# Kernel tuning notes

Measured on AMD Instinct MI355X. Metric: run time of the kernel, lower is better.

Reference implementation:

```python
import jax, jax.numpy as jnp
import numpy as np

B, S, DIM = 2, 2048, 2048
H = 16
KV_RANK = 512          # rank_lora_kv
NOPE, ROPE, VDIM = 128, 64, 128
QK = NOPE + ROPE       # 192
SCALE = QK ** -0.5     # seq <= original_seq_len so YaRN mscale = 1
THETA = 10000.0


def setup_inputs() -> dict:
    key = jax.random.key(0)
    ks = jax.random.split(key, 6)
    def w(k, shape):
        return jax.random.normal(k, shape, jnp.float32) * 0.02
    # RoPE tables (interleaved complex-pair convention, as torch.view_as_complex)
    inv = 1.0 / (THETA ** (np.arange(0, ROPE, 2, dtype=np.float32) / ROPE))
    ang = np.outer(np.arange(S, dtype=np.float32), inv)  # [S, ROPE//2]
    return {
        "x": jax.random.normal(ks[0], (B, S, DIM), jnp.float32),
        "wq": w(ks[1], (H * QK, DIM)),
        "wkv_a": w(ks[2], (KV_RANK + ROPE, DIM)),
        "kv_norm_w": jnp.ones((KV_RANK,), jnp.float32),
        "wkv_b": w(ks[3], (H * (NOPE + VDIM), KV_RANK)),
        "wo": w(ks[4], (DIM, H * VDIM)),
        "cos": jnp.asarray(np.cos(ang), jnp.float32),
        "sin": jnp.asarray(np.sin(ang), jnp.float32),
    }


def rope(x, cos, sin):
    # x: [B, S, H, ROPE]; complex-pair rotation on interleaved (even, odd) lanes
    xr = x.reshape(*x.shape[:-1], -1, 2)
    xe, xo = xr[..., 0], xr[..., 1]
    c = cos[None, :, None, :]
    s = sin[None, :, None, :]
    ye = xe * c - xo * s
    yo = xe * s + xo * c
    return jnp.stack([ye, yo], axis=-1).reshape(x.shape)


def rmsnorm(x, w, eps=1e-6):
    return x * jax.lax.rsqrt(jnp.mean(x * x, axis=-1, keepdims=True) + eps) * w


def reference(x, wq, wkv_a, kv_norm_w, wkv_b, wo, cos, sin):
    Bn, Sn, _ = x.shape
    # Q projection (q_lora_rank == 0 -> direct), split nope / rope parts
    q = (x @ wq.T).reshape(Bn, Sn, H, QK)
    q_nope, q_pe = q[..., :NOPE], q[..., NOPE:]
    q_pe = rope(q_pe, cos, sin)
    # compressed KV + decoupled shared k_pe
    kv = x @ wkv_a.T                                   # [B,S,KV_RANK+ROPE]
    c_kv, k_pe = kv[..., :KV_RANK], kv[..., KV_RANK:]
    k_pe = rope(k_pe[:, :, None, :], cos, sin)[:, :, 0, :]  # [B,S,ROPE]
    c_kv = rmsnorm(c_kv, kv_norm_w)                    # latent "KV cache" [B,S,KV_RANK]
    # absorption: fold per-head wkv_b into Q / output instead of materializing K,V
    wb = wkv_b.reshape(H, NOPE + VDIM, KV_RANK)
    wb_k, wb_v = wb[:, :NOPE], wb[:, NOPE:]
    q_lat = jnp.einsum("bshd,hdc->bshc", q_nope, wb_k)  # [B,S,H,KV_RANK]
    scores = (jnp.einsum("bshc,btc->bsht", q_lat, c_kv)
              + jnp.einsum("bshr,btr->bsht", q_pe, k_pe)) * SCALE
    causal = jnp.tril(jnp.ones((Sn, Sn), bool))
    scores = jnp.where(causal[None, :, None, :], scores, -jnp.inf)
    probs = jax.nn.softmax(scores, axis=-1)
    o_lat = jnp.einsum("bsht,btc->bshc", probs, c_kv)   # values in latent space
    o = jnp.einsum("bshc,hdc->bshd", o_lat, wb_v)       # [B,S,H,VDIM]
    return o.reshape(Bn, Sn, H * VDIM) @ wo.T
```

## Files before the change

### kernel.cpp

```cpp
#include <hip/hip_runtime.h>
#include <hip/hip_bf16.h>

typedef __hip_bfloat16 bf16;
typedef __attribute__((ext_vector_type(8))) short short8;
typedef __attribute__((ext_vector_type(4))) float f32x4;

#define S_TOK   2048
#define NROWS   4096
#define NH      16
#define QKD     192
#define NOPE_   128
#define ROPE_   64
#define VDIM_   128
#define RANK    512
#define SCALE_F 0.07216878364870323f
#define NEG_BIG -3.0e38f
#define DEFER_THR 8.0f

__device__ __forceinline__ float bl(unsigned u){ union{unsigned i; float f;} t; t.i = u << 16; return t.f; }
__device__ __forceinline__ float bh(unsigned u){ union{unsigned i; float f;} t; t.i = u & 0xffff0000u; return t.f; }
__device__ __forceinline__ unsigned short f2b(float f){
  bf16 h = __float2bfloat16(f);
  return *reinterpret_cast<unsigned short*>(&h);
}
__device__ __forceinline__ void store4(bf16* p, float a, float b, float c, float d){
  ushort4 u; u.x=f2b(a); u.y=f2b(b); u.z=f2b(c); u.w=f2b(d);
  *(ushort4*)p = u;
}
union U8 { uint4 u; short8 s; };
#define MFMA16x32(a,b,c) __builtin_amdgcn_mfma_f32_16x16x32_bf16(a,b,c,0,0,0)

__device__ __forceinline__ void gload16(const unsigned short* g, unsigned short* l)
{
  __builtin_amdgcn_global_load_lds(
      (const __attribute__((address_space(1))) unsigned int*)g,
      (__attribute__((address_space(3))) unsigned int*)l,
      16, 0, 0);
}

__global__ __launch_bounds__(256) void cvt_bf16(const float* __restrict__ src,
                                                bf16* __restrict__ dst, int n)
{
  int g = (blockIdx.x * 256 + threadIdx.x) * 4;
  if (g < n) {
    float4 v = *(const float4*)(src + g);
    store4(dst + g, v.x, v.y, v.z, v.w);
  }
}

__global__ __launch_bounds__(256) void wbhalf_cvt(const float* __restrict__ wkvb,
                                                  bf16* __restrict__ dst, int rowoff)
{
  int g = blockIdx.x * 256 + threadIdx.x;
  int h = g >> 16, rem = g & 65535;
  int d = rem >> 9, c = rem & 511;
  ((unsigned short*)dst)[g] = f2b(wkvb[((long)(h*256 + rowoff + d))*512 + c]);
}

template<typename TOUT>
__global__ __launch_bounds__(256) void gemm_mfma(
    const bf16* __restrict__ A, const bf16* __restrict__ W, TOUT* __restrict__ C,
    int K, int lda, int ldw, int ldc, long azs, long wzs, long czs)
{
  A += (long)blockIdx.z * azs;
  W += (long)blockIdx.z * wzs;
  C += (long)blockIdx.z * czs;
  __shared__ __align__(16) unsigned short As[8*65*8];
  __shared__ __align__(16) unsigned short Ws[8*65*8];
  const int tid = threadIdx.x;
  const int m0 = blockIdx.y << 6, n0 = blockIdx.x << 6;
  const int w = tid >> 6, lane = tid & 63;
  const int quad = lane >> 4, l16 = lane & 15;

  const int r0 = tid >> 3, c80 = tid & 7;
  const int r1 = (tid + 256) >> 3;

  f32x4 acc[4];
  #pragma unroll
  for (int i = 0; i < 4; ++i) acc[i] = (f32x4){0.f,0.f,0.f,0.f};

  for (int k0 = 0; k0 < K; k0 += 64) {
    uint4 a0 = *(const uint4*)(A + (long)(m0 + r0)*lda + k0 + c80*8);
    uint4 a1 = *(const uint4*)(A + (long)(m0 + r1)*lda + k0 + c80*8);
    uint4 w0 = *(const uint4*)(W + (long)(n0 + r0)*ldw + k0 + c80*8);
    uint4 w1 = *(const uint4*)(W + (long)(n0 + r1)*ldw + k0 + c80*8);
    __syncthreads();
    *(uint4*)(As + (c80*65 + r0)*8) = a0;
    *(uint4*)(As + (c80*65 + r1)*8) = a1;
    *(uint4*)(Ws + (c80*65 + r0)*8) = w0;
    *(uint4*)(Ws + (c80*65 + r1)*8) = w1;
    __syncthreads();
    #pragma unroll
    for (int kc = 0; kc < 2; ++kc) {
      const int kcq = kc*4 + quad;
      U8 af; af.u = *(const uint4*)(As + (kcq*65 + w*16 + l16)*8);
      #pragma unroll
      for (int nt = 0; nt < 4; ++nt) {
        U8 bf_; bf_.u = *(const uint4*)(Ws + (kcq*65 + nt*16 + l16)*8);
        acc[nt] = MFMA16x32(af.s, bf_.s, acc[nt]);
      }
    }
  }
  #pragma unroll
  for (int nt = 0; nt < 4; ++nt) {
    #pragma unroll
    for (int i = 0; i < 4; ++i) {
      long row = m0 + w*16 + quad*4 + i;
      TOUT v;
      if constexpr (sizeof(TOUT) == 2) v = __float2bfloat16(acc[nt][i]);
      else                             v = acc[nt][i];
      C[row*ldc + n0 + nt*16 + l16] = v;
    }
  }
}

template<typename TOUT>
__global__ __launch_bounds__(256) void gemm128(
    const bf16* __restrict__ A, const bf16* __restrict__ W, TOUT* __restrict__ C,
    int K, int lda, int ldw, int ldc, long azs, long wzs, long czs)
{
  const unsigned short* Au = (const unsigned short*)A + (long)blockIdx.z * azs;
  const unsigned short* Wu = (const unsigned short*)W + (long)blockIdx.z * wzs;
  C += (long)blockIdx.z * czs;
  __shared__ __align__(16) unsigned short smem[2048 * 8];
  const int tid = threadIdx.x;
  const int m0 = blockIdx.y << 7, n0 = blockIdx.x << 7;
  const int w = tid >> 6, lane = tid & 63;
  const int quad = lane >> 4, l16 = lane & 15;
  const int wr = w >> 1, wc = w & 1;

  f32x4 acc[4][4];
  #pragma unroll
  for (int mt = 0; mt < 4; ++mt)
    #pragma unroll
    for (int nt = 0; nt < 4; ++nt) acc[mt][nt] = (f32x4){0.f,0.f,0.f,0.f};

  for (int k0 = 0; k0 < K; k0 += 64) {
    #pragma unroll
    for (int j = 0; j < 4; ++j) {
      const int u = tid + j*256;
      const int row = u >> 3, c8 = (u & 7) ^ (row & 7);
      gload16(Au + (long)(m0 + row)*lda + k0 + c8*8, smem + (j*256 + w*64)*8);
    }
    #pragma unroll
    for (int j = 0; j < 4; ++j) {
      const int u = tid + j*256;
      const int row = u >> 3, c8 = (u & 7) ^ (row & 7);
      gload16(Wu + (long)(n0 + row)*ldw + k0 + c8*8, smem + (1024 + j*256 + w*64)*8);
    }
    __syncthreads();
    #pragma unroll
    for (int kc = 0; kc < 2; ++kc) {
      const int kcq = kc*4 + quad;
      U8 af[4];
      #pragma unroll
      for (int mt = 0; mt < 4; ++mt) {
        const int row = wr*64 + mt*16 + l16;
        af[mt].u = *(const uint4*)(smem + (row*8 + (kcq ^ (row & 7)))*8);
      }
      #pragma unroll
      for (int nt = 0; nt < 4; ++nt) {
        const int rowb = wc*64 + nt*16 + l16;
        U8 bf_; bf_.u = *(const uint4*)(smem + (1024 + rowb*8 + (kcq ^ (rowb & 7)))*8);
        #pragma unroll
        for (int mt = 0; mt < 4; ++mt)
          acc[mt][nt] = MFMA16x32(af[mt].s, bf_.s, acc[mt][nt]);
      }
    }
    __syncthreads();
  }
  #pragma unroll
  for (int mt = 0; mt < 4; ++mt) {
    #pragma unroll
    for (int nt = 0; nt < 4; ++nt) {
      #pragma unroll
      for (int i = 0; i < 4; ++i) {
        long row = m0 + wr*64 + mt*16 + quad*4 + i;
        int  col = n0 + wc*64 + nt*16 + l16;
        TOUT v;
        if constexpr (sizeof(TOUT) == 2) v = __float2bfloat16(acc[mt][nt][i]);
        else                             v = acc[mt][nt][i];
        C[row*ldc + col] = v;
      }
    }
  }
}

__global__ __launch_bounds__(64) void kvprep(
    const bf16* __restrict__ kvbuf, const float* __restrict__ wnorm,
    const float* __restrict__ cosb, const float* __restrict__ sinb,
    bf16* __restrict__ ckv, bf16* __restrict__ kpe)
{
  const int row = blockIdx.x;
  const int s = row & (S_TOK - 1);
  const int lane = threadIdx.x;
  const unsigned short* kr = (const unsigned short*)kvbuf + (long)row * 576;
  uint4 u = *(const uint4*)(kr + lane*8);
  float v[8] = { bl(u.x), bh(u.x), bl(u.y), bh(u.y), bl(u.z), bh(u.z), bl(u.w), bh(u.w) };
  float ss = 0.f;
  #pragma unroll
  for (int j = 0; j < 8; ++j) ss += v[j]*v[j];
  #pragma unroll
  for (int off = 32; off > 0; off >>= 1) ss += __shfl_down(ss, off);
  ss = __shfl(ss, 0);
  const float scl = rsqrtf(ss * (1.0f/512.0f) + 1e-6f);
  float4 w0 = *(const float4*)(wnorm + lane*8);
  float4 w1 = *(const float4*)(wnorm + lane*8 + 4);
  bf16* cd = ckv + (long)row*512 + lane*8;
  store4(cd,   v[0]*scl*w0.x, v[1]*scl*w0.y, v[2]*scl*w0.z, v[3]*scl*w0.w);
  store4(cd+4, v[4]*scl*w1.x, v[5]*scl*w1.y, v[6]*scl*w1.z, v[7]*scl*w1.w);
  if (lane < 32) {
    unsigned pe = *(const unsigned*)(kr + 512 + 2*lane);
    float xe = bl(pe), xo = bh(pe);
    float c = cosb[s*32 + lane], sn = sinb[s*32 + lane];
    ushort2 o; o.x = f2b(xe*c - xo*sn); o.y = f2b(xe*sn + xo*c);
    *(ushort2*)((unsigned short*)kpe + (long)row*64 + 2*lane) = o;
  }
}

__global__ __launch_bounds__(256) void kpe_bcast(const bf16* __restrict__ kpe,
                                                 bf16* __restrict__ khbuf)
{
  int gid = blockIdx.x * 256 + threadIdx.x;
  int row = gid >> 9; int rem = gid & 511;
  int h = rem >> 5, i = rem & 31;
  unsigned pe = *(const unsigned*)((const unsigned short*)kpe + (long)row*64 + 2*i);
  *(unsigned*)((unsigned short*)khbuf + (long)row*3072 + h*192 + 128 + 2*i) = pe;
}

__global__ __launch_bounds__(256) void ropeq(
    bf16* __restrict__ qbuf, const float* __restrict__ cosb,
    const float* __restrict__ sinb)
{
  int gid = blockIdx.x * 256 + threadIdx.x;
  int row = gid >> 9; int rem = gid & 511;
  int h = rem >> 5, i = rem & 31;
  int s = row & (S_TOK - 1);
  unsigned short* p = (unsigned short*)qbuf + (long)row*3072 + h*QKD + NOPE_ + 2*i;
  unsigned pp = *(const unsigned*)p;
  float xe = bl(pp), xo = bh(pp);
  float c = cosb[s*32 + i], sn = sinb[s*32 + i];
  ushort2 u; u.x = f2b(xe*c - xo*sn); u.y = f2b(xe*sn + xo*c);
  *(ushort2*)p = u;
}

__global__ __launch_bounds__(256) void tr_v(const bf16* __restrict__ vbuf,
                                            bf16* __restrict__ vT)
{
  const int t0 = blockIdx.x << 6, d0 = blockIdx.y << 6;
  const int b = blockIdx.z >> 4, h = blockIdx.z & 15;
  const int tid = threadIdx.x;
  __shared__ unsigned short tile[64*65];
  #pragma unroll
  for (int j = 0; j < 16; ++j) {
    int idx = tid + j*256; int r = idx >> 6, c = idx & 63;
    tile[r*65 + c] = ((const unsigned short*)vbuf)[((long)(b*S_TOK + t0 + r))*2048 + h*128 + d0 + c];
  }
  __syncthreads();
  #pragma unroll
  for (int j = 0; j < 16; ++j) {
    int idx = tid + j*256; int r = idx >> 6, t = idx & 63;
    int tt = t0 + t;
    int d  = d0 + r;
    long g = (long)(b*16 + h)*32768 + (long)(tt >> 5)*512 + d*4 + (((tt & 31) >> 3) ^ ((d >> 1) & 3));
    ((unsigned short*)vT)[g*8 + (tt & 7)] = tile[t*65 + r];
  }
}

__global__ __launch_bounds__(256, 3) void attn_mfma(
    const bf16* __restrict__ qbuf,
    const bf16* __restrict__ khbuf,
    const bf16* __restrict__ vT,
    bf16* __restrict__ obuf)
{
  const int phys = blockIdx.x;
  const int b  = (phys & 7) >> 2;
  const int r_ = ((phys & 3) << 7) | (phys >> 3);
  const int h  = r_ >> 5;
  const int qt = r_ & 31;
  const int q0 = qt << 6;
  const int tid = threadIdx.x;
  const int w = tid >> 6, lane = tid & 63;
  const int quad = lane >> 4, l16 = lane & 15;

  __shared__ __align__(16) unsigned short smem[2560 * 8];
  __shared__ __align__(16) unsigned short P_s[4 * 16 * 72];

  const unsigned short* kh_b = (const unsigned short*)khbuf + (long)b*S_TOK*3072 + h*192;
  const unsigned short* vt_b = (const unsigned short*)vT + (long)(b*16 + h)*32768*8;
  unsigned short* Pw = P_s + w*1152;

  const long qrow = (long)b*S_TOK + q0 + w*16 + l16;
  short8 qf[6];
  {
    const unsigned short* qlp = (const unsigned short*)qbuf + qrow*3072 + h*192 + quad*8;
    #pragma unroll
    for (int kc = 0; kc < 6; ++kc) { U8 t; t.u = *(const uint4*)(qlp + kc*32); qf[kc] = t.s; }
  }

  f32x4 acc[8];
  #pragma unroll
  for (int i = 0; i < 8; ++i) acc[i] = (f32x4){0.f,0.f,0.f,0.f};
  float mi[4] = {NEG_BIG,NEG_BIG,NEG_BIG,NEG_BIG};
  float li[4] = {0.f,0.f,0.f,0.f};

  const int ntiles = qt + 1;

  #pragma unroll 1
  for (int tile = 0; tile < ntiles; ++tile) {
    const int t0 = tile << 6;
    #pragma unroll
    for (int j = 0; j < 6; ++j) {
      const int u = tid + j*256;
      const int t = u / 24, c8p = u - t*24;
      const int c8 = (c8p < 16) ? ((c8p & 8) | ((c8p ^ t) & 7))
                                : (16 + ((c8p ^ t) & 7));
      gload16(kh_b + (long)(t0 + t)*3072 + c8*8, smem + (j*256 + w*64)*8);
    }
    #pragma unroll
    for (int j = 0; j < 4; ++j) {
      const unsigned short* vt = vt_b + (long)(2*tile + (j >> 1)) * 512 * 8;
      const int u = (tid + j*256) & 511;
      gload16(vt + (long)u*8, smem + (1536 + j*256 + w*64)*8);
    }
    __syncthreads();

    f32x4 sc0 = (f32x4){0.f,0.f,0.f,0.f}, sc1 = sc0, sc2 = sc0, sc3 = sc0;
    #pragma unroll
    for (int kc = 0; kc < 6; ++kc) {
      const int kcq = kc*4 + quad;
      const int sw = (kcq < 16) ? ((kcq & 8) | ((kcq ^ l16) & 7))
                                : (16 + ((kcq ^ l16) & 7));
      U8 b0; b0.u = *(const uint4*)(smem + ((     l16)*24 + sw)*8);
      U8 b1; b1.u = *(const uint4*)(smem + ((16 + l16)*24 + sw)*8);
      U8 b2; b2.u = *(const uint4*)(smem + ((32 + l16)*24 + sw)*8);
      U8 b3; b3.u = *(const uint4*)(smem + ((48 + l16)*24 + sw)*8);
      sc0 = MFMA16x32(qf[kc], b0.s, sc0);
      sc1 = MFMA16x32(qf[kc], b1.s, sc1);
      sc2 = MFMA16x32(qf[kc], b2.s, sc2);
      sc3 = MFMA16x32(qf[kc], b3.s, sc3);
    }
    float sv0[4], sv1[4], sv2[4], sv3[4], tm[4];
    #pragma unroll
    for (int i = 0; i < 4; ++i) {
      int qg = q0 + w*16 + quad*4 + i;
      sv0[i] = (t0      + l16 <= qg) ? sc0[i]*SCALE_F : NEG_BIG;
      sv1[i] = (t0 + 16 + l16 <= qg) ? sc1[i]*SCALE_F : NEG_BIG;
      sv2[i] = (t0 + 32 + l16 <= qg) ? sc2[i]*SCALE_F : NEG_BIG;
      sv3[i] = (t0 + 48 + l16 <= qg) ? sc3[i]*SCALE_F : NEG_BIG;
      tm[i] = fmaxf(fmaxf(sv0[i], sv1[i]), fmaxf(sv2[i], sv3[i]));
    }
    #pragma unroll
    for (int d = 1; d < 16; d <<= 1) {
      #pragma unroll
      for (int i = 0; i < 4; ++i) tm[i] = fmaxf(tm[i], __shfl_xor(tm[i], d));
    }
    bool small = (tm[0] - mi[0] <= DEFER_THR) && (tm[1] - mi[1] <= DEFER_THR)
              && (tm[2] - mi[2] <= DEFER_THR) && (tm[3] - mi[3] <= DEFER_THR);
    if (!__all(small)) {
      float al[4];
      #pragma unroll
      for (int i = 0; i < 4; ++i) {
        float mx = fmaxf(mi[i], tm[i]);
        al[i] = __expf(mi[i] - mx);
        mi[i] = mx;
        li[i] *= al[i];
      }
      #pragma unroll
      for (int nt = 0; nt < 8; ++nt) {
        #pragma unroll
        for (int i = 0; i < 4; ++i) acc[nt][i] *= al[i];
      }
    }
    float rs[4];
    #pragma unroll
    for (int i = 0; i < 4; ++i) {
      float p0 = __expf(sv0[i] - mi[i]);
      float p1 = __expf(sv1[i] - mi[i]);
      float p2 = __expf(sv2[i] - mi[i]);
      float p3 = __expf(sv3[i] - mi[i]);
      rs[i] = (p0 + p1) + (p2 + p3);
      const int rb = (quad*4+i)*72 + l16;
      Pw[rb]      = f2b(p0);
      Pw[rb + 16] = f2b(p1);
      Pw[rb + 32] = f2b(p2);
      Pw[rb + 48] = f2b(p3);
    }
    #pragma unroll
    for (int d = 1; d < 16; d <<= 1) {
      #pragma unroll
      for (int i = 0; i < 4; ++i) rs[i] += __shfl_xor(rs[i], d);
    }
    #pragma unroll
    for (int i = 0; i < 4; ++i) li[i] += rs[i];
    #pragma unroll
    for (int half = 0; half < 2; ++half) {
      U8 ap; ap.u = *(const uint4*)(Pw + l16*72 + half*32 + quad*8);
      #pragma unroll
      for (int nt = 0; nt < 8; ++nt) {
        const int c = nt*16 + l16;
        U8 bv; bv.u = *(const uint4*)(smem +
                       (1536 + half*512 + c*4 + (quad ^ ((c >> 1) & 3)))*8);
        acc[nt] = MFMA16x32(ap.s, bv.s, acc[nt]);
      }
    }
    __syncthreads();
  }

  float linv[4];
  #pragma unroll
  for (int i = 0; i < 4; ++i) linv[i] = 1.0f / li[i];
  #pragma unroll
  for (int nt = 0; nt < 8; ++nt) {
    #pragma unroll
    for (int i = 0; i < 4; ++i)
      ((unsigned short*)obuf)[((long)b*S_TOK + q0 + w*16 + quad*4 + i)*2048
                              + h*128 + nt*16 + l16] = f2b(acc[nt][i] * linv[i]);
  }
}

extern "C" void kernel_launch(void* const* d_in, const int* in_sizes, int n_in,
                              void* d_out, int out_size, void* d_ws, size_t ws_size,
                              hipStream_t stream)
{
  const float* x     = (const float*)d_in[0];
  const float* wq    = (const float*)d_in[1];
  const float* wkv_a = (const float*)d_in[2];
  const float* kvnw  = (const float*)d_in[3];
  const float* wkv_b = (const float*)d_in[4];
  const float* wo    = (const float*)d_in[5];
  const float* cosb  = (const float*)d_in[6];
  const float* sinb  = (const float*)d_in[7];
  float* out = (float*)d_out;

  size_t off = 0;
  char* wsb = (char*)d_ws;
  bf16* xb    = (bf16*)(wsb + off); off += (size_t)NROWS * 2048 * 2;
  bf16* wqb   = (bf16*)(wsb + off); off += (size_t)3072 * 2048 * 2;
  bf16* wab   = (bf16*)(wsb + off); off += (size_t)576  * 2048 * 2;
  bf16* wob   = (bf16*)(wsb + off); off += (size_t)2048 * 2048 * 2;
  bf16* wbkb  = (bf16*)(wsb + off); off += (size_t)1048576 * 2;
  bf16* wbvb  = (bf16*)(wsb + off); off += (size_t)1048576 * 2;
  bf16* qbuf  = (bf16*)(wsb + off); off += (size_t)NROWS * 3072 * 2;
  bf16* kvbuf = (bf16*)(wsb + off); off += (size_t)NROWS * 576  * 2;
  bf16* ckvb  = (bf16*)(wsb + off); off += (size_t)NROWS * 512  * 2;
  bf16* kpeb  = (bf16*)(wsb + off); off += (size_t)NROWS * 64   * 2;
  bf16* khbuf = (bf16*)(wsb + off); off += (size_t)NROWS * 3072 * 2;
  bf16* vbuf  = (bf16*)(wsb + off); off += (size_t)NROWS * 2048 * 2;
  bf16* vTb   = (bf16*)(wsb + off); off += (size_t)NROWS * 2048 * 2;
  bf16* obuf  = (bf16*)(wsb + off); off += (size_t)NROWS * 2048 * 2;

  dim3 blk(256);
  cvt_bf16<<<dim3(8388608/1024),  blk, 0, stream>>>(x,     xb,  8388608);
  cvt_bf16<<<dim3(6291456/1024),  blk, 0, stream>>>(wq,    wqb, 6291456);
  cvt_bf16<<<dim3(1179648/1024),  blk, 0, stream>>>(wkv_a, wab, 1179648);
  cvt_bf16<<<dim3(4194304/1024),  blk, 0, stream>>>(wo,    wob, 4194304);
  wbhalf_cvt<<<dim3(4096), blk, 0, stream>>>(wkv_b, wbkb, 0);
  wbhalf_cvt<<<dim3(4096), blk, 0, stream>>>(wkv_b, wbvb, NOPE_);
  gemm128<bf16><<<dim3(3072/128, NROWS/128, 1), blk, 0, stream>>>(
      xb, wqb, qbuf, 2048, 2048, 2048, 3072, 0, 0, 0);
  ropeq<<<dim3(8192), blk, 0, stream>>>(qbuf, cosb, sinb);
  gemm_mfma<bf16><<<dim3(576/64, NROWS/64, 1), blk, 0, stream>>>(
      xb, wab, kvbuf, 2048, 2048, 2048, 576, 0, 0, 0);
  kvprep<<<dim3(NROWS), dim3(64), 0, stream>>>(kvbuf, kvnw, cosb, sinb, ckvb, kpeb);
  kpe_bcast<<<dim3(8192), blk, 0, stream>>>(kpeb, khbuf);
  gemm128<bf16><<<dim3(1, NROWS/128, NH), blk, 0, stream>>>(
      ckvb, wbkb, khbuf, 512, 512, 512, 3072, 0, (long)128*512, (long)192);
  gemm128<bf16><<<dim3(1, NROWS/128, NH), blk, 0, stream>>>(
      ckvb, wbvb, vbuf, 512, 512, 512, 2048, 0, (long)128*512, (long)128);
  tr_v<<<dim3(S_TOK/64, 2, 32), blk, 0, stream>>>(vbuf, vTb);
  attn_mfma<<<dim3(1024), blk, 0, stream>>>(qbuf, khbuf, vTb, obuf);
  gemm128<float><<<dim3(2048/128, NROWS/128, 1), blk, 0, stream>>>(
      obuf, wob, out, 2048, 2048, 2048, 2048, 0, 0, 0);
}
```

Measured before the change: 456.5 us.

## Fuse K/V up-projection GEMMs and read shared k_pe directly in attention

Converts the full wkv_b weight with one contiguous bf16 cast and runs a single 4096-wide GEMM that writes interleaved K-nope and V per head. This replaces two per-head batched GEMMs, the strided weight-split kernels and the k_pe broadcast kernel. The attention kernel now loads the rope part of K straight from the shared kpe buffer. The small kv_a projection moves from the 64-tile GEMM to the 128-tile GEMM, with a column guard on stores. The tail tile of that GEMM reads weight rows past the 576-row end of its buffer, which are computed and then discarded.

```diff
diff --git a/kernel.cpp b/kernel.cpp
--- a/kernel.cpp
+++ b/kernel.cpp
@@ -48,76 +48,10 @@
   }
 }
 
-__global__ __launch_bounds__(256) void wbhalf_cvt(const float* __restrict__ wkvb,
-                                                  bf16* __restrict__ dst, int rowoff)
-{
-  int g = blockIdx.x * 256 + threadIdx.x;
-  int h = g >> 16, rem = g & 65535;
-  int d = rem >> 9, c = rem & 511;
-  ((unsigned short*)dst)[g] = f2b(wkvb[((long)(h*256 + rowoff + d))*512 + c]);
-}
-
-template<typename TOUT>
-__global__ __launch_bounds__(256) void gemm_mfma(
-    const bf16* __restrict__ A, const bf16* __restrict__ W, TOUT* __restrict__ C,
-    int K, int lda, int ldw, int ldc, long azs, long wzs, long czs)
-{
-  A += (long)blockIdx.z * azs;
-  W += (long)blockIdx.z * wzs;
-  C += (long)blockIdx.z * czs;
-  __shared__ __align__(16) unsigned short As[8*65*8];
-  __shared__ __align__(16) unsigned short Ws[8*65*8];
-  const int tid = threadIdx.x;
-  const int m0 = blockIdx.y << 6, n0 = blockIdx.x << 6;
-  const int w = tid >> 6, lane = tid & 63;
-  const int quad = lane >> 4, l16 = lane & 15;
-
-  const int r0 = tid >> 3, c80 = tid & 7;
-  const int r1 = (tid + 256) >> 3;
-
-  f32x4 acc[4];
-  #pragma unroll
-  for (int i = 0; i < 4; ++i) acc[i] = (f32x4){0.f,0.f,0.f,0.f};
-
-  for (int k0 = 0; k0 < K; k0 += 64) {
-    uint4 a0 = *(const uint4*)(A + (long)(m0 + r0)*lda + k0 + c80*8);
-    uint4 a1 = *(const uint4*)(A + (long)(m0 + r1)*lda + k0 + c80*8);
-    uint4 w0 = *(const uint4*)(W + (long)(n0 + r0)*ldw + k0 + c80*8);
-    uint4 w1 = *(const uint4*)(W + (long)(n0 + r1)*ldw + k0 + c80*8);
-    __syncthreads();
-    *(uint4*)(As + (c80*65 + r0)*8) = a0;
-    *(uint4*)(As + (c80*65 + r1)*8) = a1;
-    *(uint4*)(Ws + (c80*65 + r0)*8) = w0;
-    *(uint4*)(Ws + (c80*65 + r1)*8) = w1;
-    __syncthreads();
-    #pragma unroll
-    for (int kc = 0; kc < 2; ++kc) {
-      const int kcq = kc*4 + quad;
-      U8 af; af.u = *(const uint4*)(As + (kcq*65 + w*16 + l16)*8);
-      #pragma unroll
-      for (int nt = 0; nt < 4; ++nt) {
-        U8 bf_; bf_.u = *(const uint4*)(Ws + (kcq*65 + nt*16 + l16)*8);
-        acc[nt] = MFMA16x32(af.s, bf_.s, acc[nt]);
-      }
-    }
-  }
-  #pragma unroll
-  for (int nt = 0; nt < 4; ++nt) {
-    #pragma unroll
-    for (int i = 0; i < 4; ++i) {
-      long row = m0 + w*16 + quad*4 + i;
-      TOUT v;
-      if constexpr (sizeof(TOUT) == 2) v = __float2bfloat16(acc[nt][i]);
-      else                             v = acc[nt][i];
-      C[row*ldc + n0 + nt*16 + l16] = v;
-    }
-  }
-}
-
 template<typename TOUT>
 __global__ __launch_bounds__(256) void gemm128(
     const bf16* __restrict__ A, const bf16* __restrict__ W, TOUT* __restrict__ C,
-    int K, int lda, int ldw, int ldc, long azs, long wzs, long czs)
+    int K, int lda, int ldw, int ldc, int Ncols, long azs, long wzs, long czs)
 {
   const unsigned short* Au = (const unsigned short*)A + (long)blockIdx.z * azs;
   const unsigned short* Wu = (const unsigned short*)W + (long)blockIdx.z * wzs;
@@ -173,14 +107,16 @@
   for (int mt = 0; mt < 4; ++mt) {
     #pragma unroll
     for (int nt = 0; nt < 4; ++nt) {
-      #pragma unroll
-      for (int i = 0; i < 4; ++i) {
-        long row = m0 + wr*64 + mt*16 + quad*4 + i;
-        int  col = n0 + wc*64 + nt*16 + l16;
-        TOUT v;
-        if constexpr (sizeof(TOUT) == 2) v = __float2bfloat16(acc[mt][nt][i]);
-        else                             v = acc[mt][nt][i];
-        C[row*ldc + col] = v;
+      const int col = n0 + wc*64 + nt*16 + l16;
+      if (col < Ncols) {
+        #pragma unroll
+        for (int i = 0; i < 4; ++i) {
+          long row = m0 + wr*64 + mt*16 + quad*4 + i;
+          TOUT v;
+          if constexpr (sizeof(TOUT) == 2) v = __float2bfloat16(acc[mt][nt][i]);
+          else                             v = acc[mt][nt][i];
+          C[row*ldc + col] = v;
+        }
       }
     }
   }
@@ -218,16 +154,6 @@
   }
 }
 
-__global__ __launch_bounds__(256) void kpe_bcast(const bf16* __restrict__ kpe,
-                                                 bf16* __restrict__ khbuf)
-{
-  int gid = blockIdx.x * 256 + threadIdx.x;
-  int row = gid >> 9; int rem = gid & 511;
-  int h = rem >> 5, i = rem & 31;
-  unsigned pe = *(const unsigned*)((const unsigned short*)kpe + (long)row*64 + 2*i);
-  *(unsigned*)((unsigned short*)khbuf + (long)row*3072 + h*192 + 128 + 2*i) = pe;
-}
-
 __global__ __launch_bounds__(256) void ropeq(
     bf16* __restrict__ qbuf, const float* __restrict__ cosb,
     const float* __restrict__ sinb)
@@ -244,7 +170,7 @@
   *(ushort2*)p = u;
 }
 
-__global__ __launch_bounds__(256) void tr_v(const bf16* __restrict__ vbuf,
+__global__ __launch_bounds__(256) void tr_v(const bf16* __restrict__ khv,
                                             bf16* __restrict__ vT)
 {
   const int t0 = blockIdx.x << 6, d0 = blockIdx.y << 6;
@@ -254,7 +180,8 @@
   #pragma unroll
   for (int j = 0; j < 16; ++j) {
     int idx = tid + j*256; int r = idx >> 6, c = idx & 63;
-    tile[r*65 + c] = ((const unsigned short*)vbuf)[((long)(b*S_TOK + t0 + r))*2048 + h*128 + d0 + c];
+    tile[r*65 + c] = ((const unsigned short*)khv)[((long)(b*S_TOK + t0 + r))*4096
+                                                  + h*256 + 128 + d0 + c];
   }
   __syncthreads();
   #pragma unroll
@@ -269,7 +196,8 @@
 
 __global__ __launch_bounds__(256, 3) void attn_mfma(
     const bf16* __restrict__ qbuf,
-    const bf16* __restrict__ khbuf,
+    const bf16* __restrict__ khv,
+    const bf16* __restrict__ kpe,
     const bf16* __restrict__ vT,
     bf16* __restrict__ obuf)
 {
@@ -286,8 +214,9 @@
   __shared__ __align__(16) unsigned short smem[2560 * 8];
   __shared__ __align__(16) unsigned short P_s[4 * 16 * 72];
 
-  const unsigned short* kh_b = (const unsigned short*)khbuf + (long)b*S_TOK*3072 + h*192;
-  const unsigned short* vt_b = (const unsigned short*)vT + (long)(b*16 + h)*32768*8;
+  const unsigned short* kh_b  = (const unsigned short*)khv + (long)b*S_TOK*4096 + h*256;
+  const unsigned short* kpe_b = (const unsigned short*)kpe + (long)b*S_TOK*64;
+  const unsigned short* vt_b  = (const unsigned short*)vT + (long)(b*16 + h)*32768*8;
   unsigned short* Pw = P_s + w*1152;
 
   const long qrow = (long)b*S_TOK + q0 + w*16 + l16;
@@ -313,9 +242,11 @@
     for (int j = 0; j < 6; ++j) {
       const int u = tid + j*256;
       const int t = u / 24, c8p = u - t*24;
-      const int c8 = (c8p < 16) ? ((c8p & 8) | ((c8p ^ t) & 7))
-                                : (16 + ((c8p ^ t) & 7));
-      gload16(kh_b + (long)(t0 + t)*3072 + c8*8, smem + (j*256 + w*64)*8);
+      const int cK = (c8p & 8) | ((c8p ^ t) & 7);
+      const int cP = (c8p ^ t) & 7;
+      const unsigned short* srcK = kh_b  + (long)(t0 + t)*4096 + cK*8;
+      const unsigned short* srcP = kpe_b + (long)(t0 + t)*64   + cP*8;
+      gload16((c8p < 16) ? srcK : srcP, smem + (j*256 + w*64)*8);
     }
     #pragma unroll
     for (int j = 0; j < 4; ++j) {
@@ -439,37 +370,31 @@
   bf16* wqb   = (bf16*)(wsb + off); off += (size_t)3072 * 2048 * 2;
   bf16* wab   = (bf16*)(wsb + off); off += (size_t)576  * 2048 * 2;
   bf16* wob   = (bf16*)(wsb + off); off += (size_t)2048 * 2048 * 2;
-  bf16* wbkb  = (bf16*)(wsb + off); off += (size_t)1048576 * 2;
-  bf16* wbvb  = (bf16*)(wsb + off); off += (size_t)1048576 * 2;
+  bf16* wkvbb = (bf16*)(wsb + off); off += (size_t)4096 * 512 * 2;
   bf16* qbuf  = (bf16*)(wsb + off); off += (size_t)NROWS * 3072 * 2;
   bf16* kvbuf = (bf16*)(wsb + off); off += (size_t)NROWS * 576  * 2;
   bf16* ckvb  = (bf16*)(wsb + off); off += (size_t)NROWS * 512  * 2;
   bf16* kpeb  = (bf16*)(wsb + off); off += (size_t)NROWS * 64   * 2;
-  bf16* khbuf = (bf16*)(wsb + off); off += (size_t)NROWS * 3072 * 2;
-  bf16* vbuf  = (bf16*)(wsb + off); off += (size_t)NROWS * 2048 * 2;
+  bf16* khv   = (bf16*)(wsb + off); off += (size_t)NROWS * 4096 * 2;
   bf16* vTb   = (bf16*)(wsb + off); off += (size_t)NROWS * 2048 * 2;
   bf16* obuf  = (bf16*)(wsb + off); off += (size_t)NROWS * 2048 * 2;
 
   dim3 blk(256);
-  cvt_bf16<<<dim3(8388608/1024),  blk, 0, stream>>>(x,     xb,  8388608);
-  cvt_bf16<<<dim3(6291456/1024),  blk, 0, stream>>>(wq,    wqb, 6291456);
-  cvt_bf16<<<dim3(1179648/1024),  blk, 0, stream>>>(wkv_a, wab, 1179648);
-  cvt_bf16<<<dim3(4194304/1024),  blk, 0, stream>>>(wo,    wob, 4194304);
-  wbhalf_cvt<<<dim3(4096), blk, 0, stream>>>(wkv_b, wbkb, 0);
-  wbhalf_cvt<<<dim3(4096), blk, 0, stream>>>(wkv_b, wbvb, NOPE_);
+  cvt_bf16<<<dim3(8388608/1024),  blk, 0, stream>>>(x,     xb,    8388608);
+  cvt_bf16<<<dim3(6291456/1024),  blk, 0, stream>>>(wq,    wqb,   6291456);
+  cvt_bf16<<<dim3(1179648/1024),  blk, 0, stream>>>(wkv_a, wab,   1179648);
+  cvt_bf16<<<dim3(4194304/1024),  blk, 0, stream>>>(wo,    wob,   4194304);
+  cvt_bf16<<<dim3(2097152/1024),  blk, 0, stream>>>(wkv_b, wkvbb, 2097152);
   gemm128<bf16><<<dim3(3072/128, NROWS/128, 1), blk, 0, stream>>>(
-      xb, wqb, qbuf, 2048, 2048, 2048, 3072, 0, 0, 0);
+      xb, wqb, qbuf, 2048, 2048, 2048, 3072, 3072, 0, 0, 0);
   ropeq<<<dim3(8192), blk, 0, stream>>>(qbuf, cosb, sinb);
-  gemm_mfma<bf16><<<dim3(576/64, NROWS/64, 1), blk, 0, stream>>>(
-      xb, wab, kvbuf, 2048, 2048, 2048, 576, 0, 0, 0);
+  gemm128<bf16><<<dim3(5, NROWS/128, 1), blk, 0, stream>>>(
+      xb, wab, kvbuf, 2048, 2048, 2048, 576, 576, 0, 0, 0);
   kvprep<<<dim3(NROWS), dim3(64), 0, stream>>>(kvbuf, kvnw, cosb, sinb, ckvb, kpeb);
-  kpe_bcast<<<dim3(8192), blk, 0, stream>>>(kpeb, khbuf);
-  gemm128<bf16><<<dim3(1, NROWS/128, NH), blk, 0, stream>>>(
-      ckvb, wbkb, khbuf, 512, 512, 512, 3072, 0, (long)128*512, (long)192);
-  gemm128<bf16><<<dim3(1, NROWS/128, NH), blk, 0, stream>>>(
-      ckvb, wbvb, vbuf, 512, 512, 512, 2048, 0, (long)128*512, (long)128);
-  tr_v<<<dim3(S_TOK/64, 2, 32), blk, 0, stream>>>(vbuf, vTb);
-  attn_mfma<<<dim3(1024), blk, 0, stream>>>(qbuf, khbuf, vTb, obuf);
+  gemm128<bf16><<<dim3(4096/128, NROWS/128, 1), blk, 0, stream>>>(
+      ckvb, wkvbb, khv, 512, 512, 512, 4096, 4096, 0, 0, 0);
+  tr_v<<<dim3(S_TOK/64, 2, 32), blk, 0, stream>>>(khv, vTb);
+  attn_mfma<<<dim3(1024), blk, 0, stream>>>(qbuf, khv, kpeb, vTb, obuf);
   gemm128<float><<<dim3(2048/128, NROWS/128, 1), blk, 0, stream>>>(
-      obuf, wob, out, 2048, 2048, 2048, 2048, 0, 0, 0);
-}
+      obuf, wob, out, 2048, 2048, 2048, 2048, 2048, 0, 0, 0);
+}
```

Result: faster. 442.0 us (-3.2%).
